# Kernel tuning notes

Hardware: AMD Instinct MI355X
Metric: run time of the kernel (lower is better)

The kernel has to match this reference:

```python
import math
import jax, jax.numpy as jnp
import numpy as np

B, TP, E, H, HKV, D, M = 4, 8192, 4096, 32, 8, 128, 256
OUTLIERS = 8  # outlier_count_general
ROPE_THETA = 10000.0


def rotate_half(x):
    h = x.shape[-1] // 2
    return jnp.concatenate([-x[..., h:], x[..., :h]], axis=-1)


def setup_inputs() -> dict:
    key = jax.random.key(0)
    ks = jax.random.split(key, 9)
    hidden_states = jax.random.normal(ks[0], (B, 1, E), jnp.float32)
    # rotary embedding for the single new token at position TP
    inv_freq = 1.0 / (ROPE_THETA ** (np.arange(0, D, 2, dtype=np.float32) / D))
    ang = np.float32(TP) * inv_freq  # [D/2]
    cos = jnp.broadcast_to(jnp.asarray(np.concatenate([np.cos(ang), np.cos(ang)]), jnp.float32)[None, None, :], (B, 1, D))
    sin = jnp.broadcast_to(jnp.asarray(np.concatenate([np.sin(ang), np.sin(ang)]), jnp.float32)[None, None, :], (B, 1, D))
    past_keys = jax.random.normal(ks[1], (B, HKV, TP, D), jnp.float32)
    past_values = jax.random.normal(ks[2], (B, HKV, TP, D), jnp.float32)
    attention_mask = jnp.ones((B, TP + 1), jnp.float32)
    sc = E ** -0.5
    Wq = jax.random.normal(ks[3], (H * D, E), jnp.float32) * sc
    Wk = jax.random.normal(ks[4], (HKV * D, E), jnp.float32) * sc
    Wv = jax.random.normal(ks[5], (HKV * D, E), jnp.float32) * sc
    Wo = jax.random.normal(ks[6], (E, H * D), jnp.float32) * sc
    S_proj = jax.random.normal(ks[7], (D, M), jnp.float32)  # JL sketch matrix, shared across heads
    return {"hidden_states": hidden_states, "cos": cos, "sin": sin,
            "past_keys": past_keys, "past_values": past_values,
            "attention_mask": attention_mask,
            "Wq": Wq, "Wk": Wk, "Wv": Wv, "Wo": Wo, "S_proj": S_proj}


def reference(hidden_states, cos, sin, past_keys, past_values, attention_mask, Wq, Wk, Wv, Wo, S_proj):
    b = hidden_states.shape[0]
    d = past_keys.shape[-1]
    hkv = past_keys.shape[1]
    h = Wq.shape[0] // d
    g = h // hkv  # num_key_value_groups
    m = S_proj.shape[-1]

    # projections (decode step, q_len == 1)
    q = (hidden_states @ Wq.T).reshape(b, 1, h, d).transpose(0, 2, 1, 3)    # [b,H,1,d]
    k = (hidden_states @ Wk.T).reshape(b, 1, hkv, d).transpose(0, 2, 1, 3)  # [b,Hkv,1,d]
    v = (hidden_states @ Wv.T).reshape(b, 1, hkv, d).transpose(0, 2, 1, 3)

    # rotary
    c = cos[:, None, :, :]  # [b,1,1,d]
    s = sin[:, None, :, :]
    q = q * c + rotate_half(q) * s
    k = k * c + rotate_half(k) * s

    # update_sketch: append new key; keys held as raw values, quantized below
    keys = jnp.concatenate([past_keys, k], axis=2)      # [b,Hkv,T,d]
    values = jnp.concatenate([past_values, v], axis=2)  # [b,Hkv,T,d]

    # outlier channels: top-|.| channels per (batch, kv-head) kept exact
    ch_score = jnp.mean(jnp.abs(keys), axis=2)          # [b,Hkv,d]
    _, idx = jax.lax.top_k(ch_score, OUTLIERS)
    omask = jnp.sum(jax.nn.one_hot(idx, d, dtype=keys.dtype), axis=-2)  # [b,Hkv,d] in {0,1}

    # QJL 1-bit quantization of inlier part: store sign(S^T k_in) and ||k_in||
    k_in = keys * (1.0 - omask)[:, :, None, :]
    norms = jnp.linalg.norm(k_in, axis=-1)              # [b,Hkv,T]
    signs = jnp.sign(jnp.einsum('bktd,dm->bktm', k_in, S_proj))  # [b,Hkv,T,m]

    # attention_score: unbiased estimator q.k ~ ||k|| * sqrt(pi/2)/m * <S q, sign(S k)>
    qg = q[:, :, 0, :].reshape(b, hkv, g, d)            # group queries by kv head
    q_in = qg * (1.0 - omask)[:, :, None, :]
    q_out = qg * omask[:, :, None, :]
    qs = jnp.einsum('bkgd,dm->bkgm', q_in, S_proj)
    est = jnp.einsum('bkgm,bktm->bkgt', qs, signs) * (math.sqrt(math.pi / 2.0) / m) * norms[:, :, None, :]
    exact = jnp.einsum('bkgd,bktd->bkgt', q_out, keys)  # outlier channels kept full precision
    attn = (est + exact) / math.sqrt(d)                 # [b,Hkv,G,T]

    attn = attn + (1.0 - attention_mask)[:, None, None, :] * jnp.finfo(attn.dtype).min
    w = jax.nn.softmax(attn, axis=-1)

    out = jnp.einsum('bkgt,bktd->bkgd', w, values).reshape(b, 1, h * d)
    return out @ Wo.T  # [b,1,E]
```

## Files before the change

### kernel.cpp

```cpp
#include <hip/hip_runtime.h>
#include <math.h>

#define BB 4
#define TP 8192
#define TT 8193
#define EE 4096
#define HH 32
#define HKV 8
#define DD 128
#define MM 256
#define GG 4
#define NSEG 48
#define ESPLIT 8
#define TB 64
#define NT2 129
#define TCH 256
#define WCH 33

#define CJL 0.0048957583420918762f
#define RSQRT_D 0.08838834764831845f
#define NEG_HUGE -3.402823466e38f

#define KSTR 136
#define SSTR 276

typedef _Float16 f16x8 __attribute__((ext_vector_type(8)));
typedef _Float16 f16x4 __attribute__((ext_vector_type(4)));
typedef float f32x4 __attribute__((ext_vector_type(4)));

#define OFF_Q      0
#define OFF_KN     16384
#define OFF_VN     20480
#define OFF_MASKF  24576
#define OFF_STATS  28672
#define OFF_AO     29696
#define OFF_INT    46080
#define OFF_QSF    50432
#define OFF_SFRAG  115968
#define OFF_QKVP   181504
#define OFF_SCOREP 378112
#define OFF_LOGITS 181504

#define QKV_BLKS  (NSEG * ESPLIT)
#define SCORE_BLKS (BB * HKV * 64)

__global__ __launch_bounds__(256) void k1_kernel(
    const float* __restrict__ hs, const float* __restrict__ pk,
    const float* __restrict__ Wq, const float* __restrict__ Wk,
    const float* __restrict__ Wv, const float* __restrict__ Sp,
    float* __restrict__ qkvp, float* __restrict__ scorep,
    _Float16* __restrict__ Sfhi, _Float16* __restrict__ Sflo)
{
  __shared__ float smem[3072];
  int bid = blockIdx.x, tid = threadIdx.x;
  if (bid < QKV_BLKS) {
    int c = bid & 7;
    int seg = bid >> 3;
    const float* W;
    if (seg < HH)            W = Wq + (size_t)seg * DD * EE;
    else if (seg < HH + HKV) W = Wk + (size_t)(seg - HH) * DD * EE;
    else                     W = Wv + (size_t)(seg - HH - HKV) * DD * EE;
    float* hsl  = smem;
    float* sred = smem + 2048;
    for (int i = tid; i < 4 * 512; i += 256) {
      int b = i >> 9, col = i & 511;
      hsl[i] = hs[b * EE + c * 512 + col];
    }
    __syncthreads();
    int row = tid & 127, half = tid >> 7;
    const float* wr = W + (size_t)row * EE + c * 512 + half * 256;
    float4 acc[BB];
    #pragma unroll
    for (int b = 0; b < BB; ++b) acc[b] = make_float4(0.f, 0.f, 0.f, 0.f);
    for (int j = 0; j < 256; j += 4) {
      float4 w4 = *(const float4*)(wr + j);
      #pragma unroll
      for (int b = 0; b < BB; ++b) {
        float4 a4 = *(const float4*)&hsl[b * 512 + half * 256 + j];
        acc[b].x = fmaf(w4.x, a4.x, acc[b].x);
        acc[b].y = fmaf(w4.y, a4.y, acc[b].y);
        acc[b].z = fmaf(w4.z, a4.z, acc[b].z);
        acc[b].w = fmaf(w4.w, a4.w, acc[b].w);
      }
    }
    #pragma unroll
    for (int b = 0; b < BB; ++b)
      sred[(half * BB + b) * DD + row] = (acc[b].x + acc[b].y) + (acc[b].z + acc[b].w);
    __syncthreads();
    for (int i = tid; i < BB * DD; i += 256) {
      int b = i >> 7, d = i & 127;
      qkvp[(((size_t)c * NSEG + seg) * BB + b) * DD + d] =
          sred[b * DD + d] + sred[(BB + b) * DD + d];
    }
  } else if (bid < QKV_BLKS + SCORE_BLKS) {
    int id = bid - QKV_BLKS;
    int chunk = id & 63, bk = id >> 6;
    const float* base = pk + (size_t)bk * TP * DD + (size_t)chunk * 128 * DD;
    int tsub = tid >> 5, d4 = (tid & 31) * 4;
    float4 a = make_float4(0.f, 0.f, 0.f, 0.f);
    for (int t = tsub; t < 128; t += 8) {
      float4 v = *(const float4*)(base + (size_t)t * DD + d4);
      a.x += fabsf(v.x); a.y += fabsf(v.y); a.z += fabsf(v.z); a.w += fabsf(v.w);
    }
    *(float4*)&smem[tsub * DD + d4] = a;
    __syncthreads();
    if (tid < DD) {
      float s = 0.f;
      #pragma unroll
      for (int u = 0; u < 8; ++u) s += smem[u * DD + tid];
      scorep[((size_t)chunk * BB * HKV + bk) * DD + tid] = s;
    }
  } else {
    int id = bid - QKV_BLKS - SCORE_BLKS;
    int mt = id >> 2, ks = id & 3;
    int w = tid >> 6, q = (tid >> 4) & 3, l15 = tid & 15;
    f16x8 hi, lo;
    #pragma unroll
    for (int j = 0; j < 8; ++j) {
      float s = Sp[(ks * 32 + q * 8 + j) * MM + w * 64 + mt * 16 + l15];
      _Float16 h = (_Float16)s;
      hi[j] = h;
      lo[j] = (_Float16)(s - (float)h);
    }
    *(f16x8*)&Sfhi[(size_t)(id * 256 + tid) * 8] = hi;
    *(f16x8*)&Sflo[(size_t)(id * 256 + tid) * 8] = lo;
  }
}

__global__ __launch_bounds__(256) void qkv_finalize_kernel(
    const float* __restrict__ qkvp, const float* __restrict__ cosb,
    const float* __restrict__ sinb, float* __restrict__ q_out,
    float* __restrict__ k_out, float* __restrict__ v_out)
{
  int gid = blockIdx.x * 256 + threadIdx.x;
  int b = gid / 6144;
  int r = gid - b * 6144;
  int seg = r >> 7, d = r & 127;
  float sum = 0.f;
  #pragma unroll
  for (int c = 0; c < ESPLIT; ++c)
    sum += qkvp[(((size_t)c * NSEG + seg) * BB + b) * DD + d];
  if (seg >= HH + HKV) {
    v_out[((size_t)b * HKV + (seg - HH - HKV)) * DD + d] = sum;
  } else {
    float part = 0.f;
    int dp = d ^ 64;
    #pragma unroll
    for (int c = 0; c < ESPLIT; ++c)
      part += qkvp[(((size_t)c * NSEG + seg) * BB + b) * DD + dp];
    float cc = cosb[b * DD + d], ss = sinb[b * DD + d];
    float other = (d < 64) ? -part : part;
    float rv = fmaf(sum, cc, other * ss);
    if (seg < HH) q_out[((size_t)b * HH + seg) * DD + d] = rv;
    else          k_out[((size_t)b * HKV + (seg - HH)) * DD + d] = rv;
  }
}

__global__ __launch_bounds__(128) void topk_kernel(
    const float* __restrict__ scorep, const float* __restrict__ k_new,
    float* __restrict__ maskf, int* __restrict__ pos, int* __restrict__ oidx)
{
  int bk = blockIdx.x;
  int tid = threadIdx.x;
  __shared__ float sv[DD];
  __shared__ int si[DD];
  float cur = 0.f;
  for (int c = 0; c < 64; ++c)
    cur += scorep[((size_t)c * BB * HKV + bk) * DD + tid];
  cur += fabsf(k_new[bk * DD + tid]);
  maskf[bk * DD + tid] = 1.f;
  pos[bk * DD + tid] = -1;
  for (int o = 0; o < 8; ++o) {
    sv[tid] = cur; si[tid] = tid;
    __syncthreads();
    for (int st = 64; st > 0; st >>= 1) {
      if (tid < st) {
        float a = sv[tid], c2 = sv[tid + st];
        int ia = si[tid], ic = si[tid + st];
        if (c2 > a || (c2 == a && ic < ia)) { sv[tid] = c2; si[tid] = ic; }
      }
      __syncthreads();
    }
    int mi = si[0];
    __syncthreads();
    if (tid == 0) oidx[bk * 8 + o] = mi;
    if (tid == mi) { pos[bk * DD + tid] = o; maskf[bk * DD + tid] = 0.f; cur = NEG_HUGE; }
  }
}

__global__ __launch_bounds__(256) void qs_kernel(
    const float* __restrict__ q_rope, const float* __restrict__ maskf,
    const float* __restrict__ Sp, _Float16* __restrict__ qsfT)
{
  int bkg = blockIdx.x;
  int bk = bkg >> 2, g = bkg & 3;
  int b = bk >> 3, kv = bk & 7;
  __shared__ float qin[DD];
  if (threadIdx.x < DD) {
    float qv = q_rope[((size_t)b * HH + kv * GG + g) * DD + threadIdx.x];
    qin[threadIdx.x] = qv * maskf[bk * DD + threadIdx.x];
  }
  __syncthreads();
  int m = threadIdx.x;
  float acc = 0.f;
  for (int d = 0; d < DD; ++d)
    acc = fmaf(qin[d], Sp[d * MM + m], acc);
  qsfT[((size_t)bk * 16 + g) * MM + m] = (_Float16)acc;
  if (g == 0) {
    #pragma unroll
    for (int n = 4; n < 16; ++n)
      qsfT[((size_t)bk * 16 + n) * MM + m] = (_Float16)0.f;
  }
}

__global__ __launch_bounds__(256) void logits_kernel(
    const float* __restrict__ pk, const float* __restrict__ k_new,
    const _Float16* __restrict__ Sfhi, const _Float16* __restrict__ Sflo,
    const _Float16* __restrict__ qsfT, const float* __restrict__ q_rope,
    const float* __restrict__ maskf, const float* __restrict__ amask,
    float* __restrict__ logits)
{
  __shared__ union {
    struct { _Float16 hi[TB * KSTR]; _Float16 lo[TB * KSTR]; } k;
    _Float16 ssg[TB * SSTR];
  } u;
  __shared__ float norm2[TB];
  __shared__ float exv[TB][GG];

  int bk = blockIdx.x / NT2;
  int tile = blockIdx.x % NT2;
  int b = bk >> 3, kv = bk & 7;
  int t0 = tile * TB;
  int tid = threadIdx.x;
  int l15 = tid & 15;
  int q   = (tid >> 4) & 3;
  int w   = tid >> 6;
  int mb  = w * 64;
  int d4  = (tid & 31) * 4;
  int tsub = tid >> 5;

  float4 mk4 = *(const float4*)&maskf[bk * DD + d4];
  float4 qo4[GG];
  #pragma unroll
  for (int g = 0; g < GG; ++g) {
    float4 qr = *(const float4*)&q_rope[((size_t)b * HH + kv * GG + g) * DD + d4];
    qo4[g].x = qr.x * (1.f - mk4.x);
    qo4[g].y = qr.y * (1.f - mk4.y);
    qo4[g].z = qr.z * (1.f - mk4.z);
    qo4[g].w = qr.w * (1.f - mk4.w);
  }
  float4 kvr[8];
  #pragma unroll
  for (int iter = 0; iter < 8; ++iter) {
    int tg = t0 + iter * 8 + tsub;
    const float* row = (tg < TP) ? pk + ((size_t)bk * TP + tg) * DD
                                 : k_new + (size_t)bk * DD;
    kvr[iter] = *(const float4*)(row + d4);
  }

  #pragma unroll
  for (int iter = 0; iter < 8; ++iter) {
    int tl = iter * 8 + tsub;
    int tg = t0 + tl;
    float inb = (tg <= TP) ? 1.f : 0.f;
    float kx = kvr[iter].x * inb, ky = kvr[iter].y * inb,
          kz = kvr[iter].z * inb, kw = kvr[iter].w * inb;
    float exg[GG];
    #pragma unroll
    for (int g = 0; g < GG; ++g)
      exg[g] = (qo4[g].x * kx + qo4[g].y * ky) + (qo4[g].z * kz + qo4[g].w * kw);
    float v[4] = {kx * mk4.x, ky * mk4.y, kz * mk4.z, kw * mk4.w};
    float nrm = 0.f;
    f16x4 hi4, lo4;
    #pragma unroll
    for (int j = 0; j < 4; ++j) {
      nrm = fmaf(v[j], v[j], nrm);
      _Float16 h = (_Float16)v[j];
      hi4[j] = h;
      lo4[j] = (_Float16)(v[j] - (float)h);
    }
    *(f16x4*)&u.k.hi[tl * KSTR + d4] = hi4;
    *(f16x4*)&u.k.lo[tl * KSTR + d4] = lo4;
    #pragma unroll
    for (int off = 16; off > 0; off >>= 1) {
      nrm += __shfl_xor(nrm, off);
      #pragma unroll
      for (int g = 0; g < GG; ++g) exg[g] += __shfl_xor(exg[g], off);
    }
    if ((tid & 31) == 0) {
      norm2[tl] = nrm;
      #pragma unroll
      for (int g = 0; g < GG; ++g) exv[tl][g] = exg[g];
    }
  }
  __syncthreads();

  f32x4 acc[4][4];
  #pragma unroll
  for (int ts = 0; ts < 4; ++ts)
    #pragma unroll
    for (int mt = 0; mt < 4; ++mt)
      acc[ts][mt] = (f32x4){0.f, 0.f, 0.f, 0.f};

  const f16x8* SH = (const f16x8*)Sfhi;
  const f16x8* SL = (const f16x8*)Sflo;
  #pragma unroll
  for (int ks = 0; ks < 4; ++ks) {
    f16x8 sh[4], sl[4], ah[4], al[4];
    #pragma unroll
    for (int mt = 0; mt < 4; ++mt) {
      sh[mt] = SH[(size_t)(mt * 4 + ks) * 256 + tid];
      sl[mt] = SL[(size_t)(mt * 4 + ks) * 256 + tid];
    }
    #pragma unroll
    for (int ts = 0; ts < 4; ++ts) {
      ah[ts] = *(const f16x8*)&u.k.hi[(ts * 16 + l15) * KSTR + ks * 32 + q * 8];
      al[ts] = *(const f16x8*)&u.k.lo[(ts * 16 + l15) * KSTR + ks * 32 + q * 8];
    }
    #pragma unroll
    for (int ts = 0; ts < 4; ++ts)
      #pragma unroll
      for (int mt = 0; mt < 4; ++mt) {
        acc[ts][mt] = __builtin_amdgcn_mfma_f32_16x16x32_f16(ah[ts], sh[mt], acc[ts][mt], 0, 0, 0);
        acc[ts][mt] = __builtin_amdgcn_mfma_f32_16x16x32_f16(al[ts], sh[mt], acc[ts][mt], 0, 0, 0);
        acc[ts][mt] = __builtin_amdgcn_mfma_f32_16x16x32_f16(ah[ts], sl[mt], acc[ts][mt], 0, 0, 0);
      }
  }
  __syncthreads();

  #pragma unroll
  for (int ts = 0; ts < 4; ++ts)
    #pragma unroll
    for (int mt = 0; mt < 4; ++mt)
      #pragma unroll
      for (int r = 0; r < 4; ++r) {
        int tl = ts * 16 + q * 4 + r;
        int mm = mb + mt * 16 + l15;
        u.ssg[tl * SSTR + mm] = acc[ts][mt][r] >= 0.f ? (_Float16)1.f : (_Float16)-1.f;
      }
  __syncthreads();

  f32x4 eacc = (f32x4){0.f, 0.f, 0.f, 0.f};
  const _Float16* qrow = qsfT + ((size_t)bk * 16 + l15) * MM;
  #pragma unroll
  for (int ks = 0; ks < 8; ++ks) {
    f16x8 as = *(const f16x8*)&u.ssg[(16 * w + l15) * SSTR + ks * 32 + q * 8];
    f16x8 bq = *(const f16x8*)&qrow[ks * 32 + q * 8];
    eacc = __builtin_amdgcn_mfma_f32_16x16x32_f16(as, bq, eacc, 0, 0, 0);
  }

  if (l15 < 4) {
    int g = l15;
    #pragma unroll
    for (int r = 0; r < 4; ++r) {
      int tl = 16 * w + q * 4 + r;
      int tg = t0 + tl;
      if (tg < TT) {
        float logit = fmaf(eacc[r] * CJL, sqrtf(norm2[tl]), exv[tl][g]) * RSQRT_D;
        logit += (1.f - amask[b * TT + tg]) * NEG_HUGE;
        logits[((size_t)(bk * GG + g)) * TT + tg] = logit;
      }
    }
  }
}

__global__ __launch_bounds__(256) void rowstat_kernel(
    const float* __restrict__ logits, float* __restrict__ stats,
    float* __restrict__ attn_o)
{
  int row = blockIdx.x;
  const float* L = logits + (size_t)row * TT;
  int tid = threadIdx.x;
  int lane = tid & 63, wid = tid >> 6;
  __shared__ float red[8];
  if (tid < 128) attn_o[(size_t)row * DD + tid] = 0.f;
  float mx = NEG_HUGE;
  for (int i = tid; i < TT; i += 256) mx = fmaxf(mx, L[i]);
  #pragma unroll
  for (int off = 32; off > 0; off >>= 1) mx = fmaxf(mx, __shfl_xor(mx, off));
  if (lane == 0) red[wid] = mx;
  __syncthreads();
  if (tid == 0) red[4] = fmaxf(fmaxf(red[0], red[1]), fmaxf(red[2], red[3]));
  __syncthreads();
  mx = red[4];
  float sum = 0.f;
  for (int i = tid; i < TT; i += 256) sum += __expf(L[i] - mx);
  #pragma unroll
  for (int off = 32; off > 0; off >>= 1) sum += __shfl_xor(sum, off);
  if (lane == 0) red[wid] = sum;
  __syncthreads();
  if (tid == 0) {
    float s = (red[0] + red[1]) + (red[2] + red[3]);
    stats[row * 2]     = mx;
    stats[row * 2 + 1] = 1.f / s;
  }
}

__global__ __launch_bounds__(256) void wv_kernel(
    const float* __restrict__ pv, const float* __restrict__ v_new,
    const float* __restrict__ logits, const float* __restrict__ stats,
    float* __restrict__ attn_out)
{
  __shared__ float wl[GG * TCH];
  __shared__ float red[8][GG][DD];
  int bk = blockIdx.x / WCH;
  int chunk = blockIdx.x % WCH;
  int b = bk >> 3, kv = bk & 7;
  int t0 = chunk * TCH;
  const float* wbase = logits + (size_t)bk * GG * TT;
  for (int i = threadIdx.x; i < GG * TCH; i += 256) {
    int g = i >> 8, tloc = i & (TCH - 1);
    int t = t0 + tloc;
    float mxg  = stats[(bk * GG + g) * 2];
    float invg = stats[(bk * GG + g) * 2 + 1];
    wl[i] = (t < TT) ? __expf(wbase[g * TT + t] - mxg) * invg : 0.f;
  }
  __syncthreads();
  int tsub = threadIdx.x >> 5;
  int d4 = (threadIdx.x & 31) * 4;
  int tend = (t0 + TCH < TT) ? t0 + TCH : TT;
  float4 acc[GG];
  #pragma unroll
  for (int g = 0; g < GG; ++g) acc[g] = make_float4(0.f, 0.f, 0.f, 0.f);
  for (int t = t0 + tsub; t < tend; t += 8) {
    float4 v = (t < TP) ? *(const float4*)(pv + ((size_t)bk * TP + t) * DD + d4)
                        : *(const float4*)(v_new + (size_t)bk * DD + d4);
    #pragma unroll
    for (int g = 0; g < GG; ++g) {
      float wv = wl[g * TCH + (t - t0)];
      acc[g].x = fmaf(wv, v.x, acc[g].x);
      acc[g].y = fmaf(wv, v.y, acc[g].y);
      acc[g].z = fmaf(wv, v.z, acc[g].z);
      acc[g].w = fmaf(wv, v.w, acc[g].w);
    }
  }
  #pragma unroll
  for (int g = 0; g < GG; ++g) *(float4*)&red[tsub][g][d4] = acc[g];
  __syncthreads();
  if (threadIdx.x < DD) {
    int d = threadIdx.x;
    #pragma unroll
    for (int g = 0; g < GG; ++g) {
      float s = 0.f;
      #pragma unroll
      for (int ts = 0; ts < 8; ++ts) s += red[ts][g][d];
      atomicAdd(&attn_out[((size_t)b * HH + kv * GG + g) * DD + d], s);
    }
  }
}

__global__ __launch_bounds__(256) void outproj_kernel(
    const float* __restrict__ attn_out, const float* __restrict__ Wo,
    float* __restrict__ out)
{
  __shared__ float al[BB][16][260];
  int seg = blockIdx.x;
  int tid = threadIdx.x;
  for (int i = tid; i < BB * EE; i += 256) {
    int b = i >> 12, col = i & 4095;
    al[b][col >> 8][col & 255] = attn_out[(size_t)b * EE + col];
  }
  __syncthreads();
  int rloc = tid >> 4, sub = tid & 15;
  int e = seg * 16 + rloc;
  const float* wr = Wo + (size_t)e * EE + sub * 256;
  float acc[BB] = {0.f, 0.f, 0.f, 0.f};
  for (int j = 0; j < 256; j += 4) {
    float4 w4 = *(const float4*)(wr + j);
    #pragma unroll
    for (int b = 0; b < BB; ++b) {
      float4 a4 = *(const float4*)&al[b][sub][j];
      acc[b] = fmaf(w4.x, a4.x, acc[b]);
      acc[b] = fmaf(w4.y, a4.y, acc[b]);
      acc[b] = fmaf(w4.z, a4.z, acc[b]);
      acc[b] = fmaf(w4.w, a4.w, acc[b]);
    }
  }
  #pragma unroll
  for (int b = 0; b < BB; ++b) {
    acc[b] += __shfl_xor(acc[b], 1);
    acc[b] += __shfl_xor(acc[b], 2);
    acc[b] += __shfl_xor(acc[b], 4);
    acc[b] += __shfl_xor(acc[b], 8);
  }
  if (sub == 0) {
    #pragma unroll
    for (int b = 0; b < BB; ++b)
      out[(size_t)b * EE + e] = acc[b];
  }
}

extern "C" void kernel_launch(void* const* d_in, const int* in_sizes, int n_in,
                              void* d_out, int out_size, void* d_ws, size_t ws_size,
                              hipStream_t stream)
{
  const float* hs    = (const float*)d_in[0];
  const float* cosb  = (const float*)d_in[1];
  const float* sinb  = (const float*)d_in[2];
  const float* pk    = (const float*)d_in[3];
  const float* pv    = (const float*)d_in[4];
  const float* amask = (const float*)d_in[5];
  const float* Wq    = (const float*)d_in[6];
  const float* Wk    = (const float*)d_in[7];
  const float* Wv    = (const float*)d_in[8];
  const float* Wo    = (const float*)d_in[9];
  const float* Sp    = (const float*)d_in[10];
  float* out = (float*)d_out;
  float* ws = (float*)d_ws;

  float* q_rope = ws + OFF_Q;
  float* k_new  = ws + OFF_KN;
  float* v_new  = ws + OFF_VN;
  float* maskf  = ws + OFF_MASKF;
  float* stats  = ws + OFF_STATS;
  float* attn_o = ws + OFF_AO;
  int*   pos    = (int*)(ws + OFF_INT);
  int*   oidx   = pos + BB * HKV * DD;
  _Float16* qsfT = (_Float16*)(ws + OFF_QSF);
  _Float16* Sfhi = (_Float16*)(ws + OFF_SFRAG);
  _Float16* Sflo = Sfhi + 65536;
  float* qkvp   = ws + OFF_QKVP;
  float* scorep = ws + OFF_SCOREP;
  float* logits = ws + OFF_LOGITS;

  int k1_grid = QKV_BLKS + SCORE_BLKS + 16;
  k1_kernel<<<k1_grid, 256, 0, stream>>>(hs, pk, Wq, Wk, Wv, Sp,
                                         qkvp, scorep, Sfhi, Sflo);
  qkv_finalize_kernel<<<96, 256, 0, stream>>>(qkvp, cosb, sinb,
                                              q_rope, k_new, v_new);
  topk_kernel<<<BB * HKV, 128, 0, stream>>>(scorep, k_new, maskf, pos, oidx);
  qs_kernel<<<BB * HKV * GG, 256, 0, stream>>>(q_rope, maskf, Sp, qsfT);
  logits_kernel<<<BB * HKV * NT2, 256, 0, stream>>>(pk, k_new, Sfhi, Sflo, qsfT,
                                                    q_rope, maskf, amask, logits);
  rowstat_kernel<<<BB * HKV * GG, 256, 0, stream>>>(logits, stats, attn_o);
  wv_kernel<<<BB * HKV * WCH, 256, 0, stream>>>(pv, v_new, logits, stats, attn_o);
  outproj_kernel<<<256, 256, 0, stream>>>(attn_o, Wo, out);
}
```

Before: 540.1 us.

## Compute outlier exact dot and key norms via MFMA in logits kernel

The per-token exact outlier-channel dot products move from scalar FMAs plus wave shuffles into split-fp16 MFMA ops on the already-staged K tiles. Key inlier norms are now computed from the hi/lo fp16 fragments with fdot2, and the channel mask is applied as an fp16 vector multiply. The qs kernel precomputes the outlier query fragments in MFMA layout, and unused pos/oidx outputs are dropped. Launch bounds now request 3 blocks per SM, which targets higher occupancy but may cause register spills. The fp16 hi/lo split also loses some precision in the norm and exact terms.

```diff
diff --git a/kernel.cpp b/kernel.cpp
--- a/kernel.cpp
+++ b/kernel.cpp
@@ -26,6 +26,7 @@
 
 typedef _Float16 f16x8 __attribute__((ext_vector_type(8)));
 typedef _Float16 f16x4 __attribute__((ext_vector_type(4)));
+typedef _Float16 f16x2 __attribute__((ext_vector_type(2)));
 typedef float f32x4 __attribute__((ext_vector_type(4)));
 
 #define OFF_Q      0
@@ -34,12 +35,14 @@
 #define OFF_MASKF  24576
 #define OFF_STATS  28672
 #define OFF_AO     29696
-#define OFF_INT    46080
+#define OFF_MASKH  46080
 #define OFF_QSF    50432
 #define OFF_SFRAG  115968
 #define OFF_QKVP   181504
 #define OFF_SCOREP 378112
 #define OFF_LOGITS 181504
+#define OFF_QOFH   1230208
+#define OFF_QOFL   1262976
 
 #define QKV_BLKS  (NSEG * ESPLIT)
 #define SCORE_BLKS (BB * HKV * 64)
@@ -158,7 +161,7 @@
 
 __global__ __launch_bounds__(128) void topk_kernel(
     const float* __restrict__ scorep, const float* __restrict__ k_new,
-    float* __restrict__ maskf, int* __restrict__ pos, int* __restrict__ oidx)
+    float* __restrict__ maskf, _Float16* __restrict__ maskh)
 {
   int bk = blockIdx.x;
   int tid = threadIdx.x;
@@ -168,8 +171,7 @@
   for (int c = 0; c < 64; ++c)
     cur += scorep[((size_t)c * BB * HKV + bk) * DD + tid];
   cur += fabsf(k_new[bk * DD + tid]);
-  maskf[bk * DD + tid] = 1.f;
-  pos[bk * DD + tid] = -1;
+  float mf = 1.f;
   for (int o = 0; o < 8; ++o) {
     sv[tid] = cur; si[tid] = tid;
     __syncthreads();
@@ -183,14 +185,16 @@
     }
     int mi = si[0];
     __syncthreads();
-    if (tid == 0) oidx[bk * 8 + o] = mi;
-    if (tid == mi) { pos[bk * DD + tid] = o; maskf[bk * DD + tid] = 0.f; cur = NEG_HUGE; }
-  }
+    if (tid == mi) { mf = 0.f; cur = NEG_HUGE; }
+  }
+  maskf[bk * DD + tid] = mf;
+  maskh[bk * DD + tid] = (_Float16)mf;
 }
 
 __global__ __launch_bounds__(256) void qs_kernel(
     const float* __restrict__ q_rope, const float* __restrict__ maskf,
-    const float* __restrict__ Sp, _Float16* __restrict__ qsfT)
+    const float* __restrict__ Sp, _Float16* __restrict__ qsfT,
+    _Float16* __restrict__ qofh, _Float16* __restrict__ qofl)
 {
   int bkg = blockIdx.x;
   int bk = bkg >> 2, g = bkg & 3;
@@ -211,25 +215,60 @@
     for (int n = 4; n < 16; ++n)
       qsfT[((size_t)bk * 16 + n) * MM + m] = (_Float16)0.f;
   }
-}
-
-__global__ __launch_bounds__(256) void logits_kernel(
+  if (g == 1) {
+    int ks = threadIdx.x >> 6, lane = threadIdx.x & 63;
+    int qq = (lane >> 4) & 3, l15 = lane & 15;
+    f16x8 qh, ql;
+    #pragma unroll
+    for (int j = 0; j < 8; ++j) {
+      int d = ks * 32 + qq * 8 + j;
+      float val = 0.f;
+      if (l15 < 4)
+        val = q_rope[((size_t)b * HH + kv * GG + l15) * DD + d] *
+              (1.f - maskf[bk * DD + d]);
+      _Float16 h = (_Float16)val;
+      qh[j] = h;
+      ql[j] = (_Float16)(val - (float)h);
+    }
+    *(f16x8*)&qofh[((size_t)(bk * 4 + ks) * 64 + lane) * 8] = qh;
+    *(f16x8*)&qofl[((size_t)(bk * 4 + ks) * 64 + lane) * 8] = ql;
+  }
+}
+
+#if __has_builtin(__builtin_amdgcn_fdot2)
+#define NRM_STEP(P, AH, AL)                                                   \
+  {                                                                           \
+    f16x2 ph = {(AH)[2 * P], (AH)[2 * P + 1]};                                \
+    f16x2 pl = {(AL)[2 * P], (AL)[2 * P + 1]};                                \
+    nhh = __builtin_amdgcn_fdot2(ph, ph, nhh, false);                         \
+    nhl = __builtin_amdgcn_fdot2(ph, pl, nhl, false);                         \
+  }
+#else
+#define NRM_STEP(P, AH, AL)                                                   \
+  {                                                                           \
+    float h0 = (float)(AH)[2 * P], h1 = (float)(AH)[2 * P + 1];               \
+    float l0 = (float)(AL)[2 * P], l1 = (float)(AL)[2 * P + 1];               \
+    nhh = fmaf(h0, h0, fmaf(h1, h1, nhh));                                    \
+    nhl = fmaf(h0, l0, fmaf(h1, l1, nhl));                                    \
+  }
+#endif
+
+__global__ __launch_bounds__(256, 3) void logits_kernel(
     const float* __restrict__ pk, const float* __restrict__ k_new,
     const _Float16* __restrict__ Sfhi, const _Float16* __restrict__ Sflo,
-    const _Float16* __restrict__ qsfT, const float* __restrict__ q_rope,
-    const float* __restrict__ maskf, const float* __restrict__ amask,
-    float* __restrict__ logits)
+    const _Float16* __restrict__ qsfT, const _Float16* __restrict__ qofh,
+    const _Float16* __restrict__ qofl, const _Float16* __restrict__ maskh,
+    const float* __restrict__ amask, float* __restrict__ logits)
 {
   __shared__ union {
     struct { _Float16 hi[TB * KSTR]; _Float16 lo[TB * KSTR]; } k;
     _Float16 ssg[TB * SSTR];
   } u;
   __shared__ float norm2[TB];
-  __shared__ float exv[TB][GG];
 
   int bk = blockIdx.x / NT2;
   int tile = blockIdx.x % NT2;
-  int b = bk >> 3, kv = bk & 7;
+  int b = bk >> 3;
   int t0 = tile * TB;
   int tid = threadIdx.x;
   int l15 = tid & 15;
@@ -238,17 +277,8 @@
   int mb  = w * 64;
   int d4  = (tid & 31) * 4;
   int tsub = tid >> 5;
-
-  float4 mk4 = *(const float4*)&maskf[bk * DD + d4];
-  float4 qo4[GG];
-  #pragma unroll
-  for (int g = 0; g < GG; ++g) {
-    float4 qr = *(const float4*)&q_rope[((size_t)b * HH + kv * GG + g) * DD + d4];
-    qo4[g].x = qr.x * (1.f - mk4.x);
-    qo4[g].y = qr.y * (1.f - mk4.y);
-    qo4[g].z = qr.z * (1.f - mk4.z);
-    qo4[g].w = qr.w * (1.f - mk4.w);
-  }
+  int lane = tid & 63;
+
   float4 kvr[8];
   #pragma unroll
   for (int iter = 0; iter < 8; ++iter) {
@@ -257,41 +287,22 @@
                                  : k_new + (size_t)bk * DD;
     kvr[iter] = *(const float4*)(row + d4);
   }
-
   #pragma unroll
   for (int iter = 0; iter < 8; ++iter) {
     int tl = iter * 8 + tsub;
     int tg = t0 + tl;
     float inb = (tg <= TP) ? 1.f : 0.f;
-    float kx = kvr[iter].x * inb, ky = kvr[iter].y * inb,
-          kz = kvr[iter].z * inb, kw = kvr[iter].w * inb;
-    float exg[GG];
-    #pragma unroll
-    for (int g = 0; g < GG; ++g)
-      exg[g] = (qo4[g].x * kx + qo4[g].y * ky) + (qo4[g].z * kz + qo4[g].w * kw);
-    float v[4] = {kx * mk4.x, ky * mk4.y, kz * mk4.z, kw * mk4.w};
-    float nrm = 0.f;
+    float v[4] = {kvr[iter].x * inb, kvr[iter].y * inb,
+                  kvr[iter].z * inb, kvr[iter].w * inb};
     f16x4 hi4, lo4;
     #pragma unroll
     for (int j = 0; j < 4; ++j) {
-      nrm = fmaf(v[j], v[j], nrm);
       _Float16 h = (_Float16)v[j];
       hi4[j] = h;
       lo4[j] = (_Float16)(v[j] - (float)h);
     }
     *(f16x4*)&u.k.hi[tl * KSTR + d4] = hi4;
     *(f16x4*)&u.k.lo[tl * KSTR + d4] = lo4;
-    #pragma unroll
-    for (int off = 16; off > 0; off >>= 1) {
-      nrm += __shfl_xor(nrm, off);
-      #pragma unroll
-      for (int g = 0; g < GG; ++g) exg[g] += __shfl_xor(exg[g], off);
-    }
-    if ((tid & 31) == 0) {
-      norm2[tl] = nrm;
-      #pragma unroll
-      for (int g = 0; g < GG; ++g) exv[tl][g] = exg[g];
-    }
   }
   __syncthreads();
 
@@ -301,11 +312,18 @@
     #pragma unroll
     for (int mt = 0; mt < 4; ++mt)
       acc[ts][mt] = (f32x4){0.f, 0.f, 0.f, 0.f};
+  f32x4 exa = (f32x4){0.f, 0.f, 0.f, 0.f};
+  float nhh = 0.f, nhl = 0.f;
 
   const f16x8* SH = (const f16x8*)Sfhi;
   const f16x8* SL = (const f16x8*)Sflo;
+  const f16x8* QH = (const f16x8*)qofh;
+  const f16x8* QL = (const f16x8*)qofl;
   #pragma unroll
   for (int ks = 0; ks < 4; ++ks) {
+    f16x8 mA = *(const f16x8*)&maskh[bk * DD + ks * 32 + q * 8];
+    f16x8 qh = QH[(size_t)(bk * 4 + ks) * 64 + lane];
+    f16x8 ql = QL[(size_t)(bk * 4 + ks) * 64 + lane];
     f16x8 sh[4], sl[4], ah[4], al[4];
     #pragma unroll
     for (int mt = 0; mt < 4; ++mt) {
@@ -316,6 +334,28 @@
     for (int ts = 0; ts < 4; ++ts) {
       ah[ts] = *(const f16x8*)&u.k.hi[(ts * 16 + l15) * KSTR + ks * 32 + q * 8];
       al[ts] = *(const f16x8*)&u.k.lo[(ts * 16 + l15) * KSTR + ks * 32 + q * 8];
+    }
+    #pragma unroll
+    for (int ts = 0; ts < 4; ++ts) {
+      if (ts == w) {
+        exa = __builtin_amdgcn_mfma_f32_16x16x32_f16(ah[ts], qh, exa, 0, 0, 0);
+        exa = __builtin_amdgcn_mfma_f32_16x16x32_f16(al[ts], qh, exa, 0, 0, 0);
+        exa = __builtin_amdgcn_mfma_f32_16x16x32_f16(ah[ts], ql, exa, 0, 0, 0);
+      }
+    }
+    #pragma unroll
+    for (int ts = 0; ts < 4; ++ts) {
+      ah[ts] = ah[ts] * mA;
+      al[ts] = al[ts] * mA;
+    }
+    #pragma unroll
+    for (int ts = 0; ts < 4; ++ts) {
+      if (ts == w) {
+        NRM_STEP(0, ah[ts], al[ts])
+        NRM_STEP(1, ah[ts], al[ts])
+        NRM_STEP(2, ah[ts], al[ts])
+        NRM_STEP(3, ah[ts], al[ts])
+      }
     }
     #pragma unroll
     for (int ts = 0; ts < 4; ++ts)
@@ -326,6 +366,11 @@
         acc[ts][mt] = __builtin_amdgcn_mfma_f32_16x16x32_f16(ah[ts], sl[mt], acc[ts][mt], 0, 0, 0);
       }
   }
+
+  float nrm = nhh + 2.f * nhl;
+  nrm += __shfl_xor(nrm, 16);
+  nrm += __shfl_xor(nrm, 32);
+  if (q == 0) norm2[w * 16 + l15] = nrm;
   __syncthreads();
 
   #pragma unroll
@@ -356,7 +401,7 @@
       int tl = 16 * w + q * 4 + r;
       int tg = t0 + tl;
       if (tg < TT) {
-        float logit = fmaf(eacc[r] * CJL, sqrtf(norm2[tl]), exv[tl][g]) * RSQRT_D;
+        float logit = fmaf(eacc[r] * CJL, sqrtf(norm2[tl]), exa[r]) * RSQRT_D;
         logit += (1.f - amask[b * TT + tg]) * NEG_HUGE;
         logits[((size_t)(bk * GG + g)) * TT + tg] = logit;
       }
@@ -514,11 +559,12 @@
   float* maskf  = ws + OFF_MASKF;
   float* stats  = ws + OFF_STATS;
   float* attn_o = ws + OFF_AO;
-  int*   pos    = (int*)(ws + OFF_INT);
-  int*   oidx   = pos + BB * HKV * DD;
+  _Float16* maskh = (_Float16*)(ws + OFF_MASKH);
   _Float16* qsfT = (_Float16*)(ws + OFF_QSF);
   _Float16* Sfhi = (_Float16*)(ws + OFF_SFRAG);
   _Float16* Sflo = Sfhi + 65536;
+  _Float16* qofh = (_Float16*)(ws + OFF_QOFH);
+  _Float16* qofl = (_Float16*)(ws + OFF_QOFL);
   float* qkvp   = ws + OFF_QKVP;
   float* scorep = ws + OFF_SCOREP;
   float* logits = ws + OFF_LOGITS;
@@ -528,10 +574,12 @@
                                          qkvp, scorep, Sfhi, Sflo);
   qkv_finalize_kernel<<<96, 256, 0, stream>>>(qkvp, cosb, sinb,
                                               q_rope, k_new, v_new);
-  topk_kernel<<<BB * HKV, 128, 0, stream>>>(scorep, k_new, maskf, pos, oidx);
-  qs_kernel<<<BB * HKV * GG, 256, 0, stream>>>(q_rope, maskf, Sp, qsfT);
+  topk_kernel<<<BB * HKV, 128, 0, stream>>>(scorep, k_new, maskf, maskh);
+  qs_kernel<<<BB * HKV * GG, 256, 0, stream>>>(q_rope, maskf, Sp, qsfT,
+                                               qofh, qofl);
   logits_kernel<<<BB * HKV * NT2, 256, 0, stream>>>(pk, k_new, Sfhi, Sflo, qsfT,
-                                                    q_rope, maskf, amask, logits);
+                                                    qofh, qofl, maskh, amask,
+                                                    logits);
   rowstat_kernel<<<BB * HKV * GG, 256, 0, stream>>>(logits, stats, attn_o);
   wv_kernel<<<BB * HKV * WCH, 256, 0, stream>>>(pv, v_new, logits, stats, attn_o);
   outproj_kernel<<<256, 256, 0, stream>>>(attn_o, Wo, out);
```

New measurement: 505.3 us. -6.4%, faster.
